# Optimization experiments

Hardware: AMD Instinct MI355X
Metric: run time of the kernel (lower is better)

## Reference

```python
import jax, jax.numpy as jnp
import numpy as np

EMBED = 1024
B, I, J = 8, 2048, 2048
SCALE = EMBED ** -0.5


def setup_inputs() -> dict:
    key = jax.random.key(0)
    ks = jax.random.split(key, 5)
    s = EMBED ** -0.5  # init scale for weights
    return {
        "q_in": jax.random.normal(ks[0], (B, I, EMBED), dtype=jnp.float32),
        "k_v": jax.random.normal(ks[1], (B, J, EMBED), dtype=jnp.float32),
        "Wq": jax.random.normal(ks[2], (EMBED, EMBED), dtype=jnp.float32) * s,
        "bq": jnp.zeros((EMBED,), dtype=jnp.float32),
        "Wk": jax.random.normal(ks[3], (EMBED, EMBED), dtype=jnp.float32) * s,
        "bk": jnp.zeros((EMBED,), dtype=jnp.float32),
        "Wv": jax.random.normal(ks[4], (EMBED, EMBED), dtype=jnp.float32) * s,
        "bv": jnp.zeros((EMBED,), dtype=jnp.float32),
    }


def reference(q_in, k_v, Wq, bq, Wk, bk, Wv, bv):
    # Linear projections (torch Linear: x @ W.T + b; here W stored as [in, out])
    q = q_in @ Wq + bq            # [b, i, d]
    k = k_v @ Wk + bk             # [b, j, d]
    v = k_v @ Wv + bv             # [b, j, d]
    sim = jnp.einsum('bid,bjd->bij', q, k) * SCALE  # [b, i, j]
    attn = jax.nn.softmax(sim, axis=-1)
    # dropout with drop_rate=0.0 is identity
    out = jnp.einsum('bij,bjd->bid', attn, v)       # [b, i, d]
    return out
```

## Files before the change

### kernel.cpp

```cpp
#include <hip/hip_runtime.h>
#include <hip/hip_bf16.h>


#define BATCH 8
#define SEQ   2048
#define EMB   1024
#define SC2   0.045084222f

typedef __attribute__((ext_vector_type(8))) short bf16x8;
typedef __attribute__((ext_vector_type(4))) float f32x4;
typedef __attribute__((ext_vector_type(4))) unsigned short u16x4;
typedef __attribute__((ext_vector_type(8))) unsigned short u16x8;
typedef __attribute__((ext_vector_type(4))) float fl4;

__device__ __forceinline__ unsigned short f2bf(float f) {
    unsigned u = __builtin_bit_cast(unsigned, f);
    unsigned r = u + 0x7fffu + ((u >> 16) & 1u);
    return (unsigned short)(r >> 16);
}
__device__ __forceinline__ float bf2f(unsigned short s) {
    return __builtin_bit_cast(float, ((unsigned)s) << 16);
}
__device__ __forceinline__ void gload16(const unsigned short* g, unsigned short* l) {
    __builtin_amdgcn_global_load_lds(
        (const __attribute__((address_space(1))) void*)g,
        (__attribute__((address_space(3))) void*)l, 16, 0, 0);
}

__global__ __launch_bounds__(256)
void convert_in(const float* __restrict__ q_in, const float* __restrict__ k_v,
                unsigned short* __restrict__ qbin, unsigned short* __restrict__ kvbin)
{
    const size_t N = (size_t)BATCH * SEQ * EMB;
    size_t idx = ((size_t)blockIdx.x * 256 + threadIdx.x) * 8;
    const size_t stride = (size_t)gridDim.x * 256 * 8;
    for (; idx < N; idx += stride) {
        fl4 a0 = *(const fl4*)&q_in[idx];
        fl4 a1 = *(const fl4*)&q_in[idx + 4];
        fl4 b0 = *(const fl4*)&k_v[idx];
        fl4 b1 = *(const fl4*)&k_v[idx + 4];
        u16x8 ua, ub;
#pragma unroll
        for (int i = 0; i < 4; i++) {
            ua[i] = f2bf(a0[i]); ua[i + 4] = f2bf(a1[i]);
            ub[i] = f2bf(b0[i]); ub[i + 4] = f2bf(b1[i]);
        }
        *(u16x8*)&qbin[idx] = ua;
        *(u16x8*)&kvbin[idx] = ub;
    }
}

__global__ __launch_bounds__(256)
void convert_w(const float* __restrict__ Wq, const float* __restrict__ Wk,
               const float* __restrict__ Wv, unsigned short* __restrict__ Wt)
{
    const int wsel = blockIdx.y;
    const float* W = (wsel == 0) ? Wq : (wsel == 1) ? Wk : Wv;
    unsigned short* O = Wt + (size_t)wsel * EMB * EMB;
    const int k0 = (blockIdx.x >> 4) * 64;
    const int n0 = (blockIdx.x & 15) * 64;
    __shared__ unsigned short l[64 * 65];
    const int tid = threadIdx.x;
#pragma unroll
    for (int it = 0; it < 16; it++) {
        const int lin = it * 256 + tid;
        const int k = lin >> 6, n = lin & 63;
        l[n * 65 + k] = f2bf(W[(size_t)(k0 + k) * EMB + n0 + n]);
    }
    __syncthreads();
#pragma unroll
    for (int it = 0; it < 16; it++) {
        const int lin = it * 256 + tid;
        const int n = lin >> 6, k = lin & 63;
        O[(size_t)(n0 + n) * EMB + k0 + k] = l[n * 65 + k];
    }
}

__global__ __launch_bounds__(256, 2)
void proj_q_kernel(const unsigned short* __restrict__ X,
                   const unsigned short* __restrict__ Wt,
                   const float* __restrict__ bias,
                   unsigned short* __restrict__ O)
{
    const int bid = blockIdx.x;
    const int mt = ((bid >> 6) << 3) | (bid & 7);
    const int nt = (bid >> 3) & 7;
    const int m0 = mt * 128, n0 = nt * 128;

    __shared__ unsigned short lA[128 * 64];
    __shared__ unsigned short lB[128 * 64];

    const int tid = threadIdx.x, lane = tid & 63;
    const int w = tid >> 6, wr = w >> 1, wc = w & 1;
    const int r = lane & 15, g = lane >> 4;
    const int srow = lane >> 3, scol = lane & 7;

    f32x4 acc[4][4];
#pragma unroll
    for (int i = 0; i < 4; i++)
#pragma unroll
        for (int j = 0; j < 4; j++) acc[i][j] = (f32x4)0.0f;

    for (int k0 = 0; k0 < EMB; k0 += 64) {
        __syncthreads();
#pragma unroll
        for (int i = 0; i < 4; i++) {
            const int c = w * 4 + i;
            const int row = c * 8 + srow;
            gload16(&X[(size_t)(m0 + row) * EMB + k0 + scol * 8], &lA[c * 512]);
            gload16(&Wt[(size_t)(n0 + row) * EMB + k0 + scol * 8], &lB[c * 512]);
        }
        __syncthreads();
#pragma unroll
        for (int kk = 0; kk < 2; kk++) {
            bf16x8 af[4], bf[4];
#pragma unroll
            for (int m = 0; m < 4; m++)
                af[m] = *(bf16x8*)&lA[(wr * 64 + m * 16 + r) * 64 + kk * 32 + g * 8];
#pragma unroll
            for (int n = 0; n < 4; n++)
                bf[n] = *(bf16x8*)&lB[(wc * 64 + n * 16 + r) * 64 + kk * 32 + g * 8];
#pragma unroll
            for (int m = 0; m < 4; m++)
#pragma unroll
                for (int n = 0; n < 4; n++)
                    acc[m][n] = __builtin_amdgcn_mfma_f32_16x16x32_bf16(af[m], bf[n], acc[m][n], 0, 0, 0);
        }
    }

#pragma unroll
    for (int n = 0; n < 4; n++) {
        const int col = n0 + wc * 64 + n * 16 + r;
        const float bb = bias[col];
#pragma unroll
        for (int m = 0; m < 4; m++) {
            const int rowb = m0 + wr * 64 + m * 16 + g * 4;
#pragma unroll
            for (int i = 0; i < 4; i++)
                O[(size_t)(rowb + i) * EMB + col] = f2bf(acc[m][n][i] + bb);
        }
    }
}

__global__ __launch_bounds__(256, 2)
void proj_kv_kernel(const unsigned short* __restrict__ X,
                    const unsigned short* __restrict__ Wkt,
                    const unsigned short* __restrict__ Wvt,
                    const float* __restrict__ bk, const float* __restrict__ bv,
                    unsigned short* __restrict__ kb, unsigned short* __restrict__ vt)
{
    const int bid = blockIdx.x;
    const int mt = ((bid >> 6) << 3) | (bid & 7);
    const int nt = (bid >> 3) & 7;
    const int m0 = mt * 128, n0 = nt * 128;

    __shared__ unsigned short lA[128 * 64];
    __shared__ unsigned short lBk[128 * 64];
    __shared__ unsigned short lBv[128 * 64];

    const int tid = threadIdx.x, lane = tid & 63;
    const int w = tid >> 6, wr = w >> 1, wc = w & 1;
    const int r = lane & 15, g = lane >> 4;
    const int srow = lane >> 3, scol = lane & 7;

    f32x4 acck[4][4], accv[4][4];
#pragma unroll
    for (int i = 0; i < 4; i++)
#pragma unroll
        for (int j = 0; j < 4; j++) { acck[i][j] = (f32x4)0.0f; accv[i][j] = (f32x4)0.0f; }

    for (int k0 = 0; k0 < EMB; k0 += 64) {
        __syncthreads();
#pragma unroll
        for (int i = 0; i < 4; i++) {
            const int c = w * 4 + i;
            const int row = c * 8 + srow;
            const size_t goff = (size_t)row * EMB + k0 + scol * 8;
            gload16(&X[(size_t)m0 * EMB + goff], &lA[c * 512]);
            gload16(&Wkt[(size_t)n0 * EMB + goff], &lBk[c * 512]);
            gload16(&Wvt[(size_t)n0 * EMB + goff], &lBv[c * 512]);
        }
        __syncthreads();
#pragma unroll
        for (int kk = 0; kk < 2; kk++) {
            bf16x8 af[4], bfk[4], bfv[4];
#pragma unroll
            for (int m = 0; m < 4; m++)
                af[m] = *(bf16x8*)&lA[(wr * 64 + m * 16 + r) * 64 + kk * 32 + g * 8];
#pragma unroll
            for (int n = 0; n < 4; n++) {
                bfk[n] = *(bf16x8*)&lBk[(wc * 64 + n * 16 + r) * 64 + kk * 32 + g * 8];
                bfv[n] = *(bf16x8*)&lBv[(wc * 64 + n * 16 + r) * 64 + kk * 32 + g * 8];
            }
#pragma unroll
            for (int m = 0; m < 4; m++)
#pragma unroll
                for (int n = 0; n < 4; n++) {
                    acck[m][n] = __builtin_amdgcn_mfma_f32_16x16x32_bf16(af[m], bfk[n], acck[m][n], 0, 0, 0);
                    accv[m][n] = __builtin_amdgcn_mfma_f32_16x16x32_bf16(af[m], bfv[n], accv[m][n], 0, 0, 0);
                }
        }
    }

    const int b = m0 >> 11;
    const int j0 = m0 & 2047;
#pragma unroll
    for (int n = 0; n < 4; n++) {
        const int col = n0 + wc * 64 + n * 16 + r;
        const float bbk = bk[col];
        const float bbv = bv[col];
#pragma unroll
        for (int m = 0; m < 4; m++) {
            const int rowb = m0 + wr * 64 + m * 16 + g * 4;
#pragma unroll
            for (int i = 0; i < 4; i++)
                kb[(size_t)(rowb + i) * EMB + col] = f2bf(acck[m][n][i] + bbk);
            const int j = j0 + wr * 64 + m * 16 + g * 4;
            u16x4 u;
#pragma unroll
            for (int i = 0; i < 4; i++) u[i] = f2bf(accv[m][n][i] + bbv);
            *(u16x4*)&vt[((size_t)b * EMB + col) * SEQ + j] = u;
        }
    }
}

__device__ __forceinline__ void stageT(const unsigned short* lanebase, size_t rstride,
                                       unsigned short* lwave) {
#pragma unroll
    for (int i = 0; i < 2; i++)
        gload16(lanebase + (size_t)(i * 128) * rstride, lwave + i * 4096);
}

#define PIPE_PHASE1(SLOT, DO_STAGE, STAGE_A_BASE, STAGE_A_LDS)                  \
    {                                                                           \
        const unsigned short* pa = &sA[SLOT][0];                                \
        const unsigned short* pb = &sB[SLOT][0];                                \
        bf16x8 a0 = *(bf16x8*)&pa[aoff0];                                       \
        bf16x8 a1 = *(bf16x8*)&pa[aoff0 + 512];                                 \
        bf16x8 a2 = *(bf16x8*)&pa[aoff0 + 1024];                                \
        bf16x8 a3 = *(bf16x8*)&pa[aoff0 + 1536];                                \
        bv0 = *(bf16x8*)&pb[boff0];                                             \
        bv1 = *(bf16x8*)&pb[boff0 + 512];                                       \
        bv2 = *(bf16x8*)&pb[boff0 + 1024];                                      \
        bv3 = *(bf16x8*)&pb[boff0 + 1536];                                      \
        if (DO_STAGE) stageT(STAGE_A_BASE, strideA, STAGE_A_LDS);               \
        __builtin_amdgcn_s_barrier();                                           \
        asm volatile("s_waitcnt lgkmcnt(0)" ::: "memory");                      \
        __builtin_amdgcn_sched_barrier(0);                                      \
        __builtin_amdgcn_s_setprio(1);                                          \
        acc[0][0] = __builtin_amdgcn_mfma_f32_16x16x32_bf16(a0, bv0, acc[0][0], 0, 0, 0); \
        acc[0][1] = __builtin_amdgcn_mfma_f32_16x16x32_bf16(a0, bv1, acc[0][1], 0, 0, 0); \
        acc[0][2] = __builtin_amdgcn_mfma_f32_16x16x32_bf16(a0, bv2, acc[0][2], 0, 0, 0); \
        acc[0][3] = __builtin_amdgcn_mfma_f32_16x16x32_bf16(a0, bv3, acc[0][3], 0, 0, 0); \
        acc[1][0] = __builtin_amdgcn_mfma_f32_16x16x32_bf16(a1, bv0, acc[1][0], 0, 0, 0); \
        acc[1][1] = __builtin_amdgcn_mfma_f32_16x16x32_bf16(a1, bv1, acc[1][1], 0, 0, 0); \
        acc[1][2] = __builtin_amdgcn_mfma_f32_16x16x32_bf16(a1, bv2, acc[1][2], 0, 0, 0); \
        acc[1][3] = __builtin_amdgcn_mfma_f32_16x16x32_bf16(a1, bv3, acc[1][3], 0, 0, 0); \
        acc[2][0] = __builtin_amdgcn_mfma_f32_16x16x32_bf16(a2, bv0, acc[2][0], 0, 0, 0); \
        acc[2][1] = __builtin_amdgcn_mfma_f32_16x16x32_bf16(a2, bv1, acc[2][1], 0, 0, 0); \
        acc[2][2] = __builtin_amdgcn_mfma_f32_16x16x32_bf16(a2, bv2, acc[2][2], 0, 0, 0); \
        acc[2][3] = __builtin_amdgcn_mfma_f32_16x16x32_bf16(a2, bv3, acc[2][3], 0, 0, 0); \
        acc[3][0] = __builtin_amdgcn_mfma_f32_16x16x32_bf16(a3, bv0, acc[3][0], 0, 0, 0); \
        acc[3][1] = __builtin_amdgcn_mfma_f32_16x16x32_bf16(a3, bv1, acc[3][1], 0, 0, 0); \
        acc[3][2] = __builtin_amdgcn_mfma_f32_16x16x32_bf16(a3, bv2, acc[3][2], 0, 0, 0); \
        acc[3][3] = __builtin_amdgcn_mfma_f32_16x16x32_bf16(a3, bv3, acc[3][3], 0, 0, 0); \
        __builtin_amdgcn_s_setprio(0);                                          \
        __builtin_amdgcn_s_barrier();                                           \
        __builtin_amdgcn_sched_barrier(0);                                      \
    }

#define PIPE_PHASE2(SLOT, DO_STAGE, STAGE_B_BASE, STAGE_B_LDS)                  \
    {                                                                           \
        const unsigned short* pa = &sA[SLOT][0];                                \
        bf16x8 a0 = *(bf16x8*)&pa[aoff0 + 2048];                                \
        bf16x8 a1 = *(bf16x8*)&pa[aoff0 + 2560];                                \
        bf16x8 a2 = *(bf16x8*)&pa[aoff0 + 3072];                                \
        bf16x8 a3 = *(bf16x8*)&pa[aoff0 + 3584];                                \
        if (DO_STAGE) stageT(STAGE_B_BASE, strideB, STAGE_B_LDS);               \
        __builtin_amdgcn_s_barrier();                                           \
        asm volatile("s_waitcnt lgkmcnt(0)" ::: "memory");                      \
        __builtin_amdgcn_sched_barrier(0);                                      \
        __builtin_amdgcn_s_setprio(1);                                          \
        acc[4][0] = __builtin_amdgcn_mfma_f32_16x16x32_bf16(a0, bv0, acc[4][0], 0, 0, 0); \
        acc[4][1] = __builtin_amdgcn_mfma_f32_16x16x32_bf16(a0, bv1, acc[4][1], 0, 0, 0); \
        acc[4][2] = __builtin_amdgcn_mfma_f32_16x16x32_bf16(a0, bv2, acc[4][2], 0, 0, 0); \
        acc[4][3] = __builtin_amdgcn_mfma_f32_16x16x32_bf16(a0, bv3, acc[4][3], 0, 0, 0); \
        acc[5][0] = __builtin_amdgcn_mfma_f32_16x16x32_bf16(a1, bv0, acc[5][0], 0, 0, 0); \
        acc[5][1] = __builtin_amdgcn_mfma_f32_16x16x32_bf16(a1, bv1, acc[5][1], 0, 0, 0); \
        acc[5][2] = __builtin_amdgcn_mfma_f32_16x16x32_bf16(a1, bv2, acc[5][2], 0, 0, 0); \
        acc[5][3] = __builtin_amdgcn_mfma_f32_16x16x32_bf16(a1, bv3, acc[5][3], 0, 0, 0); \
        acc[6][0] = __builtin_amdgcn_mfma_f32_16x16x32_bf16(a2, bv0, acc[6][0], 0, 0, 0); \
        acc[6][1] = __builtin_amdgcn_mfma_f32_16x16x32_bf16(a2, bv1, acc[6][1], 0, 0, 0); \
        acc[6][2] = __builtin_amdgcn_mfma_f32_16x16x32_bf16(a2, bv2, acc[6][2], 0, 0, 0); \
        acc[6][3] = __builtin_amdgcn_mfma_f32_16x16x32_bf16(a2, bv3, acc[6][3], 0, 0, 0); \
        acc[7][0] = __builtin_amdgcn_mfma_f32_16x16x32_bf16(a3, bv0, acc[7][0], 0, 0, 0); \
        acc[7][1] = __builtin_amdgcn_mfma_f32_16x16x32_bf16(a3, bv1, acc[7][1], 0, 0, 0); \
        acc[7][2] = __builtin_amdgcn_mfma_f32_16x16x32_bf16(a3, bv2, acc[7][2], 0, 0, 0); \
        acc[7][3] = __builtin_amdgcn_mfma_f32_16x16x32_bf16(a3, bv3, acc[7][3], 0, 0, 0); \
        __builtin_amdgcn_s_setprio(0);                                          \
        asm volatile("s_waitcnt vmcnt(4)" ::: "memory");                        \
        __builtin_amdgcn_s_barrier();                                           \
        __builtin_amdgcn_sched_barrier(0);                                      \
    }

__global__ __launch_bounds__(512, 2)
void qk256_kernel(const unsigned short* __restrict__ qb,
                  const unsigned short* __restrict__ kb,
                  unsigned short* __restrict__ P,
                  float* __restrict__ Ppart)
{
    __shared__ unsigned short sA[4][8192];
    __shared__ unsigned short sB[4][8192];

    const int bid = blockIdx.x;
    const int lid = (bid & 7) * 64 + (bid >> 3);
    const int b = lid >> 6;
    const int mt = (lid >> 3) & 7, nt = lid & 7;
    const int m0 = mt * 256, n0 = nt * 256;
    const size_t strideA = EMB, strideB = EMB;
    const unsigned short* Ag = qb + (size_t)b * SEQ * EMB;
    const unsigned short* Bg = kb + (size_t)b * SEQ * EMB;

    const int tid = threadIdx.x, lane = tid & 63;
    const int wid = tid >> 6, wr = wid >> 2, wn = wid & 3;
    const int r = lane & 15, g = lane >> 4;

    const unsigned short* Asrc = Ag + (size_t)(m0 + (tid >> 2)) * strideA + (tid & 3) * 8;
    const unsigned short* Bsrc = Bg + (size_t)(n0 + (tid >> 2)) * strideB + (tid & 3) * 8;
    const int lwave = (wid << 9);

    const int aoff0 = (wr * 128 + r) * 32 + g * 8;
    const int boff0 = (wn * 64 + r) * 32 + g * 8;

    f32x4 acc[8][4];
#pragma unroll
    for (int i = 0; i < 8; i++)
#pragma unroll
        for (int j = 0; j < 4; j++) acc[i][j] = (f32x4)0.0f;

    const int NT = EMB / 32;

    stageT(Asrc, strideA, &sA[0][lwave]);
    stageT(Bsrc, strideB, &sB[0][lwave]);
    stageT(Asrc + 32, strideA, &sA[1][lwave]);
    stageT(Bsrc + 32, strideB, &sB[1][lwave]);
    asm volatile("s_waitcnt vmcnt(4)" ::: "memory");
    __builtin_amdgcn_s_barrier();
    __builtin_amdgcn_sched_barrier(0);

    bf16x8 bv0, bv1, bv2, bv3;
    for (int T = 0; T < NT; ++T) {
        const int s = T & 3;
        const int doStage = (T + 2 < NT);
        const int s2 = (T + 2) & 3;
        PIPE_PHASE1(s, doStage, Asrc + (T + 2) * 32, &sA[s2][lwave]);
        PIPE_PHASE2(s, doStage, Bsrc + (T + 2) * 32, &sB[s2][lwave]);
    }

    unsigned short* Pb = P + (size_t)b * SEQ * SEQ;
    float ps[8][4];
#pragma unroll
    for (int mm = 0; mm < 8; mm++)
#pragma unroll
        for (int i = 0; i < 4; i++) ps[mm][i] = 0.f;

#pragma unroll
    for (int mm = 0; mm < 8; mm++) {
        const int ib = m0 + wr * 128 + mm * 16 + g * 4;
#pragma unroll
        for (int n = 0; n < 4; n++) {
            const int j = n0 + wn * 64 + n * 16 + r;
#pragma unroll
            for (int i = 0; i < 4; i++) {
                const float p = exp2f(acc[mm][n][i] * SC2);
                ps[mm][i] += p;
                Pb[(size_t)(ib + i) * SEQ + j] = f2bf(p);
            }
        }
    }
#pragma unroll
    for (int off = 1; off < 16; off <<= 1)
#pragma unroll
        for (int mm = 0; mm < 8; mm++)
#pragma unroll
            for (int i = 0; i < 4; i++)
                ps[mm][i] += __shfl_xor(ps[mm][i], off);
    if (r == 0) {
        const int slot = nt * 4 + wn;
        float* pp = Ppart + (size_t)slot * (BATCH * SEQ) + (size_t)b * SEQ;
#pragma unroll
        for (int mm = 0; mm < 8; mm++) {
            const int row = m0 + wr * 128 + mm * 16 + g * 4;
#pragma unroll
            for (int i = 0; i < 4; i++) pp[row + i] = ps[mm][i];
        }
    }
}

__global__ __launch_bounds__(256)
void rowsum_final(const float* __restrict__ Ppart, float* __restrict__ rs)
{
    const int row = blockIdx.x * 256 + threadIdx.x;
    float s = 0.f;
#pragma unroll
    for (int slot = 0; slot < 32; slot++)
        s += Ppart[(size_t)slot * (BATCH * SEQ) + row];
    rs[row] = s;
}

__global__ __launch_bounds__(512, 2)
void pv256_kernel(const unsigned short* __restrict__ P,
                  const unsigned short* __restrict__ vt,
                  const float* __restrict__ rs,
                  float* __restrict__ out)
{
    __shared__ unsigned short sA[4][8192];
    __shared__ unsigned short sB[4][8192];

    const int bid = blockIdx.x;
    const int lid = (bid & 7) * 32 + (bid >> 3);
    const int b = lid >> 5;
    const int mt = (lid >> 2) & 7, nt = lid & 3;
    const int m0 = mt * 256, n0 = nt * 256;
    const size_t strideA = SEQ, strideB = SEQ;
    const unsigned short* Ag = P + (size_t)b * SEQ * SEQ;
    const unsigned short* Bg = vt + (size_t)b * EMB * SEQ;

    const int tid = threadIdx.x, lane = tid & 63;
    const int wid = tid >> 6, wr = wid >> 2, wn = wid & 3;
    const int r = lane & 15, g = lane >> 4;

    const unsigned short* Asrc = Ag + (size_t)(m0 + (tid >> 2)) * strideA + (tid & 3) * 8;
    const unsigned short* Bsrc = Bg + (size_t)(n0 + (tid >> 2)) * strideB + (tid & 3) * 8;
    const int lwave = (wid << 9);

    const int aoff0 = (wr * 128 + r) * 32 + g * 8;
    const int boff0 = (wn * 64 + r) * 32 + g * 8;

    f32x4 acc[8][4];
#pragma unroll
    for (int i = 0; i < 8; i++)
#pragma unroll
        for (int j = 0; j < 4; j++) acc[i][j] = (f32x4)0.0f;

    const int NT = SEQ / 32;

    stageT(Asrc, strideA, &sA[0][lwave]);
    stageT(Bsrc, strideB, &sB[0][lwave]);
    stageT(Asrc + 32, strideA, &sA[1][lwave]);
    stageT(Bsrc + 32, strideB, &sB[1][lwave]);
    asm volatile("s_waitcnt vmcnt(4)" ::: "memory");
    __builtin_amdgcn_s_barrier();
    __builtin_amdgcn_sched_barrier(0);

    bf16x8 bv0, bv1, bv2, bv3;
    for (int T = 0; T < NT; ++T) {
        const int s = T & 3;
        const int doStage = (T + 2 < NT);
        const int s2 = (T + 2) & 3;
        PIPE_PHASE1(s, doStage, Asrc + (T + 2) * 32, &sA[s2][lwave]);
        PIPE_PHASE2(s, doStage, Bsrc + (T + 2) * 32, &sB[s2][lwave]);
    }

    float* ob = out + (size_t)b * SEQ * EMB;
    const float* rsb = rs + (size_t)b * SEQ;
#pragma unroll
    for (int mm = 0; mm < 8; mm++) {
        const int ib = m0 + wr * 128 + mm * 16 + g * 4;
#pragma unroll
        for (int i = 0; i < 4; i++) {
            const float inv = 1.0f / rsb[ib + i];
#pragma unroll
            for (int n = 0; n < 4; n++) {
                const int d = n0 + wn * 64 + n * 16 + r;
                ob[(size_t)(ib + i) * EMB + d] = acc[mm][n][i] * inv;
            }
        }
    }
}

extern "C" void kernel_launch(void* const* d_in, const int* in_sizes, int n_in,
                              void* d_out, int out_size, void* d_ws, size_t ws_size,
                              hipStream_t stream)
{
    const float* q_in = (const float*)d_in[0];
    const float* k_v  = (const float*)d_in[1];
    const float* Wq   = (const float*)d_in[2];
    const float* bq   = (const float*)d_in[3];
    const float* Wk   = (const float*)d_in[4];
    const float* bk   = (const float*)d_in[5];
    const float* Wv   = (const float*)d_in[6];
    const float* bv   = (const float*)d_in[7];
    float* out = (float*)d_out;

    char* ws = (char*)d_ws;
    unsigned short* qbin = (unsigned short*)(ws);
    unsigned short* kvbin= (unsigned short*)(ws + (size_t)33554432);
    unsigned short* P    = (unsigned short*)(ws);
    unsigned short* qb   = (unsigned short*)(ws + (size_t)67108864);
    unsigned short* kb   = (unsigned short*)(ws + (size_t)100663296);
    unsigned short* vt   = (unsigned short*)(ws + (size_t)134217728);
    unsigned short* Wt   = (unsigned short*)(ws + (size_t)167772160);
    float*          Ppart= (float*)(ws + (size_t)174063616);
    float*          rs   = (float*)(ws + (size_t)176160768);

    convert_in<<<4096, 256, 0, stream>>>(q_in, k_v, qbin, kvbin);
    convert_w<<<dim3(256, 3), 256, 0, stream>>>(Wq, Wk, Wv, Wt);
    proj_q_kernel<<<1024, 256, 0, stream>>>(qbin, Wt, bq, qb);
    proj_kv_kernel<<<1024, 256, 0, stream>>>(kvbin, Wt + (size_t)EMB * EMB,
                                             Wt + (size_t)2 * EMB * EMB, bk, bv, kb, vt);
    qk256_kernel<<<512, 512, 0, stream>>>(qb, kb, P, Ppart);
    rowsum_final<<<64, 256, 0, stream>>>(Ppart, rs);
    pv256_kernel<<<256, 512, 0, stream>>>(P, vt, rs, out);
}
```

Before: 329.8 us.

## Move projections onto shared 256-tile pipelined GEMM and swap operand roles

Replaces the simple 128x128 projection kernels with the 4-stage pipelined 256x256 GEMM routine already used for attention, factored into a shared device function. Q projection and the fused K/V projection (Wk and Wv treated as one 2048-wide matrix) now use the larger tiles. QK and PV swap their A/B operands so each lane holds contiguous output columns and can write vectorized 4-element stores. The row-sum partials shrink from 32 slots to 16. Launch bounds drop to one block per SM, which trades occupancy for the larger tiles.

New measurement: 323.6 us. Within noise of the previous version (-1.9%).

```diff
diff --git a/kernel.cpp b/kernel.cpp
--- a/kernel.cpp
+++ b/kernel.cpp
@@ -73,154 +73,6 @@
         const int lin = it * 256 + tid;
         const int n = lin >> 6, k = lin & 63;
         O[(size_t)(n0 + n) * EMB + k0 + k] = l[n * 65 + k];
-    }
-}
-
-__global__ __launch_bounds__(256, 2)
-void proj_q_kernel(const unsigned short* __restrict__ X,
-                   const unsigned short* __restrict__ Wt,
-                   const float* __restrict__ bias,
-                   unsigned short* __restrict__ O)
-{
-    const int bid = blockIdx.x;
-    const int mt = ((bid >> 6) << 3) | (bid & 7);
-    const int nt = (bid >> 3) & 7;
-    const int m0 = mt * 128, n0 = nt * 128;
-
-    __shared__ unsigned short lA[128 * 64];
-    __shared__ unsigned short lB[128 * 64];
-
-    const int tid = threadIdx.x, lane = tid & 63;
-    const int w = tid >> 6, wr = w >> 1, wc = w & 1;
-    const int r = lane & 15, g = lane >> 4;
-    const int srow = lane >> 3, scol = lane & 7;
-
-    f32x4 acc[4][4];
-#pragma unroll
-    for (int i = 0; i < 4; i++)
-#pragma unroll
-        for (int j = 0; j < 4; j++) acc[i][j] = (f32x4)0.0f;
-
-    for (int k0 = 0; k0 < EMB; k0 += 64) {
-        __syncthreads();
-#pragma unroll
-        for (int i = 0; i < 4; i++) {
-            const int c = w * 4 + i;
-            const int row = c * 8 + srow;
-            gload16(&X[(size_t)(m0 + row) * EMB + k0 + scol * 8], &lA[c * 512]);
-            gload16(&Wt[(size_t)(n0 + row) * EMB + k0 + scol * 8], &lB[c * 512]);
-        }
-        __syncthreads();
-#pragma unroll
-        for (int kk = 0; kk < 2; kk++) {
-            bf16x8 af[4], bf[4];
-#pragma unroll
-            for (int m = 0; m < 4; m++)
-                af[m] = *(bf16x8*)&lA[(wr * 64 + m * 16 + r) * 64 + kk * 32 + g * 8];
-#pragma unroll
-            for (int n = 0; n < 4; n++)
-                bf[n] = *(bf16x8*)&lB[(wc * 64 + n * 16 + r) * 64 + kk * 32 + g * 8];
-#pragma unroll
-            for (int m = 0; m < 4; m++)
-#pragma unroll
-                for (int n = 0; n < 4; n++)
-                    acc[m][n] = __builtin_amdgcn_mfma_f32_16x16x32_bf16(af[m], bf[n], acc[m][n], 0, 0, 0);
-        }
-    }
-
-#pragma unroll
-    for (int n = 0; n < 4; n++) {
-        const int col = n0 + wc * 64 + n * 16 + r;
-        const float bb = bias[col];
-#pragma unroll
-        for (int m = 0; m < 4; m++) {
-            const int rowb = m0 + wr * 64 + m * 16 + g * 4;
-#pragma unroll
-            for (int i = 0; i < 4; i++)
-                O[(size_t)(rowb + i) * EMB + col] = f2bf(acc[m][n][i] + bb);
-        }
-    }
-}
-
-__global__ __launch_bounds__(256, 2)
-void proj_kv_kernel(const unsigned short* __restrict__ X,
-                    const unsigned short* __restrict__ Wkt,
-                    const unsigned short* __restrict__ Wvt,
-                    const float* __restrict__ bk, const float* __restrict__ bv,
-                    unsigned short* __restrict__ kb, unsigned short* __restrict__ vt)
-{
-    const int bid = blockIdx.x;
-    const int mt = ((bid >> 6) << 3) | (bid & 7);
-    const int nt = (bid >> 3) & 7;
-    const int m0 = mt * 128, n0 = nt * 128;
-
-    __shared__ unsigned short lA[128 * 64];
-    __shared__ unsigned short lBk[128 * 64];
-    __shared__ unsigned short lBv[128 * 64];
-
-    const int tid = threadIdx.x, lane = tid & 63;
-    const int w = tid >> 6, wr = w >> 1, wc = w & 1;
-    const int r = lane & 15, g = lane >> 4;
-    const int srow = lane >> 3, scol = lane & 7;
-
-    f32x4 acck[4][4], accv[4][4];
-#pragma unroll
-    for (int i = 0; i < 4; i++)
-#pragma unroll
-        for (int j = 0; j < 4; j++) { acck[i][j] = (f32x4)0.0f; accv[i][j] = (f32x4)0.0f; }
-
-    for (int k0 = 0; k0 < EMB; k0 += 64) {
-        __syncthreads();
-#pragma unroll
-        for (int i = 0; i < 4; i++) {
-            const int c = w * 4 + i;
-            const int row = c * 8 + srow;
-            const size_t goff = (size_t)row * EMB + k0 + scol * 8;
-            gload16(&X[(size_t)m0 * EMB + goff], &lA[c * 512]);
-            gload16(&Wkt[(size_t)n0 * EMB + goff], &lBk[c * 512]);
-            gload16(&Wvt[(size_t)n0 * EMB + goff], &lBv[c * 512]);
-        }
-        __syncthreads();
-#pragma unroll
-        for (int kk = 0; kk < 2; kk++) {
-            bf16x8 af[4], bfk[4], bfv[4];
-#pragma unroll
-            for (int m = 0; m < 4; m++)
-                af[m] = *(bf16x8*)&lA[(wr * 64 + m * 16 + r) * 64 + kk * 32 + g * 8];
-#pragma unroll
-            for (int n = 0; n < 4; n++) {
-                bfk[n] = *(bf16x8*)&lBk[(wc * 64 + n * 16 + r) * 64 + kk * 32 + g * 8];
-                bfv[n] = *(bf16x8*)&lBv[(wc * 64 + n * 16 + r) * 64 + kk * 32 + g * 8];
-            }
-#pragma unroll
-            for (int m = 0; m < 4; m++)
-#pragma unroll
-                for (int n = 0; n < 4; n++) {
-                    acck[m][n] = __builtin_amdgcn_mfma_f32_16x16x32_bf16(af[m], bfk[n], acck[m][n], 0, 0, 0);
-                    accv[m][n] = __builtin_amdgcn_mfma_f32_16x16x32_bf16(af[m], bfv[n], accv[m][n], 0, 0, 0);
-                }
-        }
-    }
-
-    const int b = m0 >> 11;
-    const int j0 = m0 & 2047;
-#pragma unroll
-    for (int n = 0; n < 4; n++) {
-        const int col = n0 + wc * 64 + n * 16 + r;
-        const float bbk = bk[col];
-        const float bbv = bv[col];
-#pragma unroll
-        for (int m = 0; m < 4; m++) {
-            const int rowb = m0 + wr * 64 + m * 16 + g * 4;
-#pragma unroll
-            for (int i = 0; i < 4; i++)
-                kb[(size_t)(rowb + i) * EMB + col] = f2bf(acck[m][n][i] + bbk);
-            const int j = j0 + wr * 64 + m * 16 + g * 4;
-            u16x4 u;
-#pragma unroll
-            for (int i = 0; i < 4; i++) u[i] = f2bf(accv[m][n][i] + bbv);
-            *(u16x4*)&vt[((size_t)b * EMB + col) * SEQ + j] = u;
-        }
     }
 }
 
@@ -303,43 +155,14 @@
         __builtin_amdgcn_sched_barrier(0);                                      \
     }
 
-__global__ __launch_bounds__(512, 2)
-void qk256_kernel(const unsigned short* __restrict__ qb,
-                  const unsigned short* __restrict__ kb,
-                  unsigned short* __restrict__ P,
-                  float* __restrict__ Ppart)
-{
-    __shared__ unsigned short sA[4][8192];
-    __shared__ unsigned short sB[4][8192];
-
-    const int bid = blockIdx.x;
-    const int lid = (bid & 7) * 64 + (bid >> 3);
-    const int b = lid >> 6;
-    const int mt = (lid >> 3) & 7, nt = lid & 7;
-    const int m0 = mt * 256, n0 = nt * 256;
-    const size_t strideA = EMB, strideB = EMB;
-    const unsigned short* Ag = qb + (size_t)b * SEQ * EMB;
-    const unsigned short* Bg = kb + (size_t)b * SEQ * EMB;
-
-    const int tid = threadIdx.x, lane = tid & 63;
-    const int wid = tid >> 6, wr = wid >> 2, wn = wid & 3;
-    const int r = lane & 15, g = lane >> 4;
-
-    const unsigned short* Asrc = Ag + (size_t)(m0 + (tid >> 2)) * strideA + (tid & 3) * 8;
-    const unsigned short* Bsrc = Bg + (size_t)(n0 + (tid >> 2)) * strideB + (tid & 3) * 8;
-    const int lwave = (wid << 9);
-
-    const int aoff0 = (wr * 128 + r) * 32 + g * 8;
-    const int boff0 = (wn * 64 + r) * 32 + g * 8;
-
-    f32x4 acc[8][4];
-#pragma unroll
-    for (int i = 0; i < 8; i++)
-#pragma unroll
-        for (int j = 0; j < 4; j++) acc[i][j] = (f32x4)0.0f;
-
-    const int NT = EMB / 32;
-
+__device__ __forceinline__ void pipe_gemm(
+    const unsigned short* __restrict__ Asrc,
+    const unsigned short* __restrict__ Bsrc,
+    const size_t strideA, const size_t strideB, const int NT,
+    unsigned short (*sA)[8192], unsigned short (*sB)[8192],
+    const int lwave, const int aoff0, const int boff0,
+    f32x4 acc[8][4])
+{
     stageT(Asrc, strideA, &sA[0][lwave]);
     stageT(Bsrc, strideB, &sB[0][lwave]);
     stageT(Asrc + 32, strideA, &sA[1][lwave]);
@@ -356,44 +179,150 @@
         PIPE_PHASE1(s, doStage, Asrc + (T + 2) * 32, &sA[s2][lwave]);
         PIPE_PHASE2(s, doStage, Bsrc + (T + 2) * 32, &sB[s2][lwave]);
     }
+}
+
+#define PIPE_PREAMBLE                                                     \
+    __shared__ unsigned short sA[4][8192];                                \
+    __shared__ unsigned short sB[4][8192];                                \
+    const int tid = threadIdx.x, lane = tid & 63;                         \
+    const int wid = tid >> 6, wr = wid >> 2, wn = wid & 3;                \
+    const int r = lane & 15, g = lane >> 4;                               \
+    const int lwave = (wid << 9);                                         \
+    const int aoff0 = (wr * 128 + r) * 32 + g * 8;                        \
+    const int boff0 = (wn * 64 + r) * 32 + g * 8;                         \
+    f32x4 acc[8][4];                                                      \
+    _Pragma("unroll") for (int i_ = 0; i_ < 8; i_++)                      \
+    _Pragma("unroll") for (int j_ = 0; j_ < 4; j_++) acc[i_][j_] = (f32x4)0.0f;
+
+__global__ __launch_bounds__(512, 1)
+void proj_q256(const unsigned short* __restrict__ Wqt,
+               const unsigned short* __restrict__ X,
+               const float* __restrict__ bias,
+               unsigned short* __restrict__ qb)
+{
+    PIPE_PREAMBLE
+    const int bid = blockIdx.x;
+    const int lid = (bid & 7) * 32 + (bid >> 3);
+    const int dt = lid & 3, it = lid >> 2;
+    const int d0 = dt * 256, i0 = it * 256;
+    const size_t strideA = EMB, strideB = EMB;
+    const unsigned short* Asrc = Wqt + (size_t)(d0 + (tid >> 2)) * EMB + (tid & 3) * 8;
+    const unsigned short* Bsrc = X + (size_t)(i0 + (tid >> 2)) * EMB + (tid & 3) * 8;
+
+    pipe_gemm(Asrc, Bsrc, strideA, strideB, EMB / 32, sA, sB, lwave, aoff0, boff0, acc);
+
+#pragma unroll
+    for (int mm = 0; mm < 8; mm++) {
+        const int dbase = d0 + wr * 128 + mm * 16 + g * 4;
+        const fl4 b4 = *(const fl4*)&bias[dbase];
+#pragma unroll
+        for (int n = 0; n < 4; n++) {
+            const int i = i0 + wn * 64 + n * 16 + r;
+            u16x4 u;
+#pragma unroll
+            for (int c = 0; c < 4; c++) u[c] = f2bf(acc[mm][n][c] + b4[c]);
+            *(u16x4*)&qb[(size_t)i * EMB + dbase] = u;
+        }
+    }
+}
+
+__global__ __launch_bounds__(512, 1)
+void proj_kv256(const unsigned short* __restrict__ X,
+                const unsigned short* __restrict__ Wkvt,
+                const float* __restrict__ bk, const float* __restrict__ bv,
+                unsigned short* __restrict__ kb, unsigned short* __restrict__ vt)
+{
+    PIPE_PREAMBLE
+    const int bid = blockIdx.x;
+    const int lid = (bid & 7) * 64 + (bid >> 3);
+    const int nt = lid & 7, mt = lid >> 3;
+    const int m0 = mt * 256, n0 = nt * 256;
+    const size_t strideA = EMB, strideB = EMB;
+    const unsigned short* Asrc = X + (size_t)(m0 + (tid >> 2)) * EMB + (tid & 3) * 8;
+    const unsigned short* Bsrc = Wkvt + (size_t)(n0 + (tid >> 2)) * EMB + (tid & 3) * 8;
+
+    pipe_gemm(Asrc, Bsrc, strideA, strideB, EMB / 32, sA, sB, lwave, aoff0, boff0, acc);
+
+    const int b = m0 >> 11;
+    const int j0l = m0 & 2047;
+    if (n0 < 1024) {
+#pragma unroll
+        for (int mm = 0; mm < 8; mm++) {
+            const int ibase = m0 + wr * 128 + mm * 16 + g * 4;
+#pragma unroll
+            for (int n = 0; n < 4; n++) {
+                const int col = n0 + wn * 64 + n * 16 + r;
+                const float bb = bk[col];
+#pragma unroll
+                for (int c = 0; c < 4; c++)
+                    kb[(size_t)(ibase + c) * EMB + col] = f2bf(acc[mm][n][c] + bb);
+            }
+        }
+    } else {
+#pragma unroll
+        for (int mm = 0; mm < 8; mm++) {
+            const int jbase = j0l + wr * 128 + mm * 16 + g * 4;
+#pragma unroll
+            for (int n = 0; n < 4; n++) {
+                const int d = n0 - 1024 + wn * 64 + n * 16 + r;
+                const float bb = bv[d];
+                u16x4 u;
+#pragma unroll
+                for (int c = 0; c < 4; c++) u[c] = f2bf(acc[mm][n][c] + bb);
+                *(u16x4*)&vt[((size_t)b * EMB + d) * SEQ + jbase] = u;
+            }
+        }
+    }
+}
+
+__global__ __launch_bounds__(512, 1)
+void qk256_kernel(const unsigned short* __restrict__ qb,
+                  const unsigned short* __restrict__ kb,
+                  unsigned short* __restrict__ P,
+                  float* __restrict__ Ppart)
+{
+    PIPE_PREAMBLE
+    const int bid = blockIdx.x;
+    const int lid = (bid & 7) * 64 + (bid >> 3);
+    const int b = lid >> 6, jt = (lid >> 3) & 7, it = lid & 7;
+    const int j0 = jt * 256, i0 = it * 256;
+    const size_t strideA = EMB, strideB = EMB;
+    const unsigned short* Ag = kb + (size_t)b * SEQ * EMB;
+    const unsigned short* Bg = qb + (size_t)b * SEQ * EMB;
+    const unsigned short* Asrc = Ag + (size_t)(j0 + (tid >> 2)) * EMB + (tid & 3) * 8;
+    const unsigned short* Bsrc = Bg + (size_t)(i0 + (tid >> 2)) * EMB + (tid & 3) * 8;
+
+    pipe_gemm(Asrc, Bsrc, strideA, strideB, EMB / 32, sA, sB, lwave, aoff0, boff0, acc);
 
     unsigned short* Pb = P + (size_t)b * SEQ * SEQ;
-    float ps[8][4];
-#pragma unroll
-    for (int mm = 0; mm < 8; mm++)
-#pragma unroll
-        for (int i = 0; i < 4; i++) ps[mm][i] = 0.f;
-
+    float ps[4] = {0.f, 0.f, 0.f, 0.f};
 #pragma unroll
     for (int mm = 0; mm < 8; mm++) {
-        const int ib = m0 + wr * 128 + mm * 16 + g * 4;
+        const int jbase = j0 + wr * 128 + mm * 16 + g * 4;
 #pragma unroll
         for (int n = 0; n < 4; n++) {
-            const int j = n0 + wn * 64 + n * 16 + r;
-#pragma unroll
-            for (int i = 0; i < 4; i++) {
-                const float p = exp2f(acc[mm][n][i] * SC2);
-                ps[mm][i] += p;
-                Pb[(size_t)(ib + i) * SEQ + j] = f2bf(p);
+            const int i = i0 + wn * 64 + n * 16 + r;
+            u16x4 u;
+#pragma unroll
+            for (int c = 0; c < 4; c++) {
+                const float p = exp2f(acc[mm][n][c] * SC2);
+                ps[n] += p;
+                u[c] = f2bf(p);
             }
-        }
-    }
-#pragma unroll
-    for (int off = 1; off < 16; off <<= 1)
-#pragma unroll
-        for (int mm = 0; mm < 8; mm++)
-#pragma unroll
-            for (int i = 0; i < 4; i++)
-                ps[mm][i] += __shfl_xor(ps[mm][i], off);
-    if (r == 0) {
-        const int slot = nt * 4 + wn;
+            *(u16x4*)&Pb[(size_t)i * SEQ + jbase] = u;
+        }
+    }
+#pragma unroll
+    for (int n = 0; n < 4; n++) {
+        ps[n] += __shfl_xor(ps[n], 16);
+        ps[n] += __shfl_xor(ps[n], 32);
+    }
+    if (g == 0) {
+        const int slot = jt * 2 + wr;
         float* pp = Ppart + (size_t)slot * (BATCH * SEQ) + (size_t)b * SEQ;
 #pragma unroll
-        for (int mm = 0; mm < 8; mm++) {
-            const int row = m0 + wr * 128 + mm * 16 + g * 4;
-#pragma unroll
-            for (int i = 0; i < 4; i++) pp[row + i] = ps[mm][i];
-        }
+        for (int n = 0; n < 4; n++)
+            pp[i0 + wn * 64 + n * 16 + r] = ps[n];
     }
 }
 
@@ -403,78 +332,46 @@
     const int row = blockIdx.x * 256 + threadIdx.x;
     float s = 0.f;
 #pragma unroll
-    for (int slot = 0; slot < 32; slot++)
+    for (int slot = 0; slot < 16; slot++)
         s += Ppart[(size_t)slot * (BATCH * SEQ) + row];
     rs[row] = s;
 }
 
-__global__ __launch_bounds__(512, 2)
+__global__ __launch_bounds__(512, 1)
 void pv256_kernel(const unsigned short* __restrict__ P,
                   const unsigned short* __restrict__ vt,
                   const float* __restrict__ rs,
                   float* __restrict__ out)
 {
-    __shared__ unsigned short sA[4][8192];
-    __shared__ unsigned short sB[4][8192];
-
+    PIPE_PREAMBLE
     const int bid = blockIdx.x;
     const int lid = (bid & 7) * 32 + (bid >> 3);
-    const int b = lid >> 5;
-    const int mt = (lid >> 2) & 7, nt = lid & 3;
-    const int m0 = mt * 256, n0 = nt * 256;
+    const int b = lid >> 5, it = (lid >> 2) & 7, dt = lid & 3;
+    const int d0 = dt * 256, i0 = it * 256;
     const size_t strideA = SEQ, strideB = SEQ;
-    const unsigned short* Ag = P + (size_t)b * SEQ * SEQ;
-    const unsigned short* Bg = vt + (size_t)b * EMB * SEQ;
-
-    const int tid = threadIdx.x, lane = tid & 63;
-    const int wid = tid >> 6, wr = wid >> 2, wn = wid & 3;
-    const int r = lane & 15, g = lane >> 4;
-
-    const unsigned short* Asrc = Ag + (size_t)(m0 + (tid >> 2)) * strideA + (tid & 3) * 8;
-    const unsigned short* Bsrc = Bg + (size_t)(n0 + (tid >> 2)) * strideB + (tid & 3) * 8;
-    const int lwave = (wid << 9);
-
-    const int aoff0 = (wr * 128 + r) * 32 + g * 8;
-    const int boff0 = (wn * 64 + r) * 32 + g * 8;
-
-    f32x4 acc[8][4];
-#pragma unroll
-    for (int i = 0; i < 8; i++)
-#pragma unroll
-        for (int j = 0; j < 4; j++) acc[i][j] = (f32x4)0.0f;
-
-    const int NT = SEQ / 32;
-
-    stageT(Asrc, strideA, &sA[0][lwave]);
-    stageT(Bsrc, strideB, &sB[0][lwave]);
-    stageT(Asrc + 32, strideA, &sA[1][lwave]);
-    stageT(Bsrc + 32, strideB, &sB[1][lwave]);
-    asm volatile("s_waitcnt vmcnt(4)" ::: "memory");
-    __builtin_amdgcn_s_barrier();
-    __builtin_amdgcn_sched_barrier(0);
-
-    bf16x8 bv0, bv1, bv2, bv3;
-    for (int T = 0; T < NT; ++T) {
-        const int s = T & 3;
-        const int doStage = (T + 2 < NT);
-        const int s2 = (T + 2) & 3;
-        PIPE_PHASE1(s, doStage, Asrc + (T + 2) * 32, &sA[s2][lwave]);
-        PIPE_PHASE2(s, doStage, Bsrc + (T + 2) * 32, &sB[s2][lwave]);
-    }
+    const unsigned short* Ag = vt + (size_t)b * EMB * SEQ;
+    const unsigned short* Bg = P + (size_t)b * SEQ * SEQ;
+    const unsigned short* Asrc = Ag + (size_t)(d0 + (tid >> 2)) * SEQ + (tid & 3) * 8;
+    const unsigned short* Bsrc = Bg + (size_t)(i0 + (tid >> 2)) * SEQ + (tid & 3) * 8;
+
+    pipe_gemm(Asrc, Bsrc, strideA, strideB, SEQ / 32, sA, sB, lwave, aoff0, boff0, acc);
 
     float* ob = out + (size_t)b * SEQ * EMB;
     const float* rsb = rs + (size_t)b * SEQ;
+    float inv[4];
+#pragma unroll
+    for (int n = 0; n < 4; n++)
+        inv[n] = 1.0f / rsb[i0 + wn * 64 + n * 16 + r];
 #pragma unroll
     for (int mm = 0; mm < 8; mm++) {
-        const int ib = m0 + wr * 128 + mm * 16 + g * 4;
-#pragma unroll
-        for (int i = 0; i < 4; i++) {
-            const float inv = 1.0f / rsb[ib + i];
-#pragma unroll
-            for (int n = 0; n < 4; n++) {
-                const int d = n0 + wn * 64 + n * 16 + r;
-                ob[(size_t)(ib + i) * EMB + d] = acc[mm][n][i] * inv;
-            }
+        const int dbase = d0 + wr * 128 + mm * 16 + g * 4;
+#pragma unroll
+        for (int n = 0; n < 4; n++) {
+            const int i = i0 + wn * 64 + n * 16 + r;
+            fl4 o;
+#pragma unroll
+            for (int c = 0; c < 4; c++) o[c] = acc[mm][n][c] * inv[n];
+            *(fl4*)&ob[(size_t)i * EMB + dbase] = o;
         }
     }
 }
@@ -502,13 +399,12 @@
     unsigned short* vt   = (unsigned short*)(ws + (size_t)134217728);
     unsigned short* Wt   = (unsigned short*)(ws + (size_t)167772160);
     float*          Ppart= (float*)(ws + (size_t)174063616);
-    float*          rs   = (float*)(ws + (size_t)176160768);
+    float*          rs   = (float*)(ws + (size_t)175112192);
 
     convert_in<<<4096, 256, 0, stream>>>(q_in, k_v, qbin, kvbin);
     convert_w<<<dim3(256, 3), 256, 0, stream>>>(Wq, Wk, Wv, Wt);
-    proj_q_kernel<<<1024, 256, 0, stream>>>(qbin, Wt, bq, qb);
-    proj_kv_kernel<<<1024, 256, 0, stream>>>(kvbin, Wt + (size_t)EMB * EMB,
-                                             Wt + (size_t)2 * EMB * EMB, bk, bv, kb, vt);
+    proj_q256<<<256, 512, 0, stream>>>(Wt, qbin, bq, qb);
+    proj_kv256<<<512, 512, 0, stream>>>(kvbin, Wt + (size_t)EMB * EMB, bk, bv, kb, vt);
     qk256_kernel<<<512, 512, 0, stream>>>(qb, kb, P, Ppart);
     rowsum_final<<<64, 256, 0, stream>>>(Ppart, rs);
     pv256_kernel<<<256, 512, 0, stream>>>(P, vt, rs, out);
```
